# Performance work log

Hardware: AMD Instinct MI355X
Metric: run time of the kernel (lower is better)

Reference implementation:

```python
import jax, jax.numpy as jnp
import numpy as np

DIM = 256
HEADS = 8
BS = 8
N = 1024
NEG = -1.0e9


def setup_inputs() -> dict:
    key = jax.random.key(0)
    ks = jax.random.split(key, 8)
    feats = jax.random.normal(ks[0], (BS, N, DIM), dtype=jnp.float32)
    adj_mat = (jax.random.uniform(ks[1], (BS, N, N)) < 0.1).astype(jnp.float32)
    s = 1.0 / np.sqrt(DIM)
    fc_w = jax.random.normal(ks[2], (DIM, DIM * HEADS), dtype=jnp.float32) * s
    fc_b = jnp.zeros((DIM * HEADS,), dtype=jnp.float32)
    q_w = jax.random.normal(ks[3], (DIM, 1), dtype=jnp.float32) * s
    q_b = jnp.zeros((1,), dtype=jnp.float32)
    k_w = jax.random.normal(ks[4], (DIM, 1), dtype=jnp.float32) * s
    k_b = jnp.zeros((1,), dtype=jnp.float32)
    fp_w = jax.random.normal(ks[5], (DIM * HEADS, DIM), dtype=jnp.float32) * (1.0 / np.sqrt(DIM * HEADS))
    fp_b = jnp.zeros((DIM,), dtype=jnp.float32)
    return {"feats": feats, "adj_mat": adj_mat, "fc_w": fc_w, "fc_b": fc_b,
            "q_w": q_w, "q_b": q_b, "k_w": k_w, "k_b": k_b,
            "fp_w": fp_w, "fp_b": fp_b}


def reference(feats, adj_mat, fc_w, fc_b, q_w, q_b, k_w, k_b, fp_w, fp_b):
    bs, n, dim = feats.shape
    # [bs, N, heads*dim] -> [bs, heads, N, dim]
    feat_proj = (feats @ fc_w + fc_b).reshape(bs, n, HEADS, dim).transpose(0, 2, 1, 3)
    q = feat_proj @ q_w + q_b            # [bs, heads, N, 1]
    k = feat_proj @ k_w + k_b            # [bs, heads, N, 1]
    logits = q + jnp.swapaxes(k, -1, -2)  # additive scores [bs, heads, N, N]
    masked = logits + (1.0 - adj_mat[:, None]) * NEG
    masked = jax.nn.leaky_relu(masked, negative_slope=0.01)
    attn = jax.nn.softmax(masked, axis=-1)  # dropout is identity at eval
    out = attn @ feat_proj                   # [bs, heads, N, dim]
    out = out.transpose(0, 2, 1, 3).reshape(bs, n, HEADS * dim)
    out = out @ fp_w + fp_b + feats          # residual=True
    return jax.nn.sigmoid(out)
```

## Files before the change

kernel.cpp:

```cpp
#include <hip/hip_runtime.h>
#include <hip/hip_bf16.h>

typedef unsigned short u16;
typedef unsigned int u32;
typedef unsigned long long u64;
typedef __attribute__((ext_vector_type(8))) short short8;
typedef __attribute__((ext_vector_type(4))) float floatx4;
typedef const __attribute__((address_space(1))) void* gp_t;
typedef __attribute__((address_space(3))) void* sp_t;

static __device__ __forceinline__ u16 f2bf(float x) {
    __hip_bfloat16 h = __float2bfloat16(x);
    union { __hip_bfloat16 h; u16 u; } cv; cv.h = h; return cv.u;
}
static __device__ __forceinline__ float bf2f(u16 u) {
    union { u16 u; __hip_bfloat16 h; } cv; cv.u = u;
    return __bfloat162float(cv.h);
}

__global__ __launch_bounds__(256)
void k_prepall(const float* __restrict__ feats, const float* __restrict__ adj,
               const float* __restrict__ fc_w, const float* __restrict__ fc_b,
               const float* __restrict__ q_w, const float* __restrict__ q_b,
               const float* __restrict__ k_w, const float* __restrict__ k_b,
               const float* __restrict__ fp_w,
               u16* __restrict__ featsB, u64* __restrict__ m,
               u16* __restrict__ fcwT, u16* __restrict__ fpwT2,
               u16* __restrict__ W, float* __restrict__ C) {
    __shared__ float shbuf[64 * 65];
    int id = blockIdx.x, tid = threadIdx.x;
    if (id < 32768) {
        long i = (long)id * 256 + tid;
        float v = adj[i];
        u64 bm = __ballot(v > 0.f);
        if ((tid & 63) == 0) m[i >> 6] = bm;
        if (id < 2048) {
            int j = (id * 256 + tid) * 4;
            float4 f = *(const float4*)&feats[j];
            featsB[j + 0] = f2bf(f.x); featsB[j + 1] = f2bf(f.y);
            featsB[j + 2] = f2bf(f.z); featsB[j + 3] = f2bf(f.w);
        }
    } else if (id < 32896) {
        int t = id - 32768, bx = t & 31, by = t >> 5;
        float (*tt)[65] = (float(*)[65])shbuf;
        int c = tid & 63, r0 = tid >> 6;
        for (int rr = r0; rr < 64; rr += 4)
            tt[rr][c] = fc_w[(long)(by * 64 + rr) * 2048 + bx * 64 + c];
        __syncthreads();
        for (int rr = r0; rr < 64; rr += 4)
            fcwT[(long)(bx * 64 + rr) * 256 + by * 64 + c] = f2bf(tt[c][rr]);
    } else if (id < 34944) {
        int k = id - 32896;
        float v = fp_w[(long)k * 256 + tid];
        fpwT2[((long)(k >> 3)) * 2048 + tid * 8 + (k & 7)] = f2bf(v);
    } else {
        int t = id - 34944, x = t & 15, dq = t >> 4;
        int h = x & 7, kind = x >> 3;
        const float* w = kind ? k_w : q_w;
        float* ws_ = shbuf;
        ws_[tid] = w[tid];
        __syncthreads();
        int dl = tid >> 2, part = tid & 3;
        int d = dq * 64 + dl;
        const float* row = fc_w + (long)d * 2048 + h * 256 + part * 64;
        float a = 0.f;
        #pragma unroll 8
        for (int i = 0; i < 64; i++) a += row[i] * ws_[part * 64 + i];
        a += __shfl_xor(a, 1);
        a += __shfl_xor(a, 2);
        if (part == 0) W[(long)x * 256 + d] = f2bf(a);
        if (tid == 0 && dq == 0) {
            float cb = 0.f;
            const float* fb = fc_b + h * 256;
            for (int i = 0; i < 256; i++) cb += fb[i] * ws_[i];
            C[x] = cb + (kind ? k_b[0] : q_b[0]);
        }
    }
}

__global__ __launch_bounds__(256, 2)
void k_g1qk(const u16* __restrict__ A, const u16* __restrict__ Bt,
            const float* __restrict__ bias, u16* __restrict__ V2,
            const u16* __restrict__ Wb, const float* __restrict__ C,
            float* __restrict__ qo, float* __restrict__ ko) {
    __shared__ u16 As[128 * 40];
    __shared__ u16 Bs[128 * 40];
    int tid  = threadIdx.x;
    int wave = tid >> 6, lane = tid & 63;
    int q  = lane >> 4, n16 = lane & 15;

    if (blockIdx.y >= 16) {
        int blk = (blockIdx.y - 16) * 64 + blockIdx.x;
        int rowBase = blk * 64 + wave * 16;
        const u16* arow = Bt + (long)(rowBase + n16) * 256 + q * 8;
        const u16* brow = Wb + n16 * 256 + q * 8;
        floatx4 acc = {};
        #pragma unroll
        for (int k0 = 0; k0 < 256; k0 += 32) {
            short8 af = *(const short8*)&arow[k0];
            short8 bf = *(const short8*)&brow[k0];
            acc = __builtin_amdgcn_mfma_f32_16x16x32_bf16(af, bf, acc, 0, 0, 0);
        }
        float cc = C[n16];
        #pragma unroll
        for (int r = 0; r < 4; r++) {
            int gr = rowBase + q * 4 + r;
            int b = gr >> 10, nn = gr & 1023;
            float v = acc[r] + cc;
            if (n16 < 8) qo[((b * 8 + n16) << 10) + nn] = v;
            else         ko[((b * 8 + (n16 - 8)) << 10) + nn] = v;
        }
        return;
    }

    int rowBase = blockIdx.y * 128;
    int colBase = blockIdx.x * 128;
    int wr = wave >> 1, wc = wave & 1;
    floatx4 acc[4][4] = {};
    int sm = tid >> 2;
    int sk = (tid & 3) * 8;

    for (int k0 = 0; k0 < 256; k0 += 32) {
        int4 a0 = *(const int4*)&A[(long)(rowBase + sm) * 256 + k0 + sk];
        int4 a1 = *(const int4*)&A[(long)(rowBase + sm + 64) * 256 + k0 + sk];
        int4 b0 = *(const int4*)&Bt[(long)(colBase + sm) * 256 + k0 + sk];
        int4 b1 = *(const int4*)&Bt[(long)(colBase + sm + 64) * 256 + k0 + sk];
        __syncthreads();
        *(int4*)&As[sm * 40 + sk]        = a0;
        *(int4*)&As[(sm + 64) * 40 + sk] = a1;
        *(int4*)&Bs[sm * 40 + sk]        = b0;
        *(int4*)&Bs[(sm + 64) * 40 + sk] = b1;
        __syncthreads();
        short8 af[4], bfr[4];
        #pragma unroll
        for (int i = 0; i < 4; i++)
            af[i] = *(short8*)&As[(wr * 64 + i * 16 + n16) * 40 + q * 8];
        #pragma unroll
        for (int i = 0; i < 4; i++)
            bfr[i] = *(short8*)&Bs[(wc * 64 + i * 16 + n16) * 40 + q * 8];
        #pragma unroll
        for (int mi = 0; mi < 4; mi++)
            #pragma unroll
            for (int ni = 0; ni < 4; ni++)
                acc[mi][ni] = __builtin_amdgcn_mfma_f32_16x16x32_bf16(
                    af[mi], bfr[ni], acc[mi][ni], 0, 0, 0);
    }

    #pragma unroll
    for (int mi = 0; mi < 4; mi++) {
        #pragma unroll
        for (int r = 0; r < 4; r++) {
            int grow = rowBase + wr * 64 + mi * 16 + q * 4 + r;
            int h = grow >> 8, d = grow & 255;
            float bv = bias[grow];
            #pragma unroll
            for (int ni = 0; ni < 4; ni++) {
                int gcol = colBase + wc * 64 + ni * 16 + n16;
                int b = gcol >> 10, nn = gcol & 1023;
                V2[(((long)(b * 8 + h)) << 18) + (nn >> 3) * 2048 + d * 8 + (nn & 7)]
                    = f2bf(acc[mi][ni][r] + bv);
            }
        }
    }
}

__global__ __launch_bounds__(512)
__attribute__((amdgpu_waves_per_eu(4)))
void k_attn(const u32* __restrict__ maskW, const float* __restrict__ qv,
            const float* __restrict__ kv, const u16* __restrict__ fpjT2,
            u16* __restrict__ outh2) {
    __shared__ u16 As[2][128 * 40];
    __shared__ u16 Bs[2][4 * 256 * 8];
    __shared__ float qS[128], kS[1024], lsumS[512], rlS[128];

    int z = blockIdx.x;
    int b = z >> 3, h = z & 7;
    int i0 = blockIdx.y * 128;
    int tid = threadIdx.x;
    int wave = tid >> 6, lane = tid & 63;
    int wr = wave >> 2, wc = wave & 3;
    int q  = lane >> 4, n16 = lane & 15;

    if (tid < 256) *(float4*)&kS[tid * 4] = *(const float4*)&kv[(z << 10) + tid * 4];
    if (tid >= 256 && tid < 384) qS[tid - 256] = qv[(z << 10) + i0 + (tid - 256)];

    floatx4 acc[4][4] = {};
    int ar = tid >> 2;
    int jq = (tid & 3) * 8;
    const u32* mrow = maskW + (((long)(b << 10) + i0 + ar) << 5);
    const u16* Vbase = fpjT2 + ((long)z << 18);
    float lsum = 0.f;

    auto dma_v = [&](int k0, int p) {
        #pragma unroll
        for (int t = 0; t < 2; t++) {
            int s = wave * 2 + t;
            __builtin_amdgcn_global_load_lds(
                (gp_t)&Vbase[((k0 >> 3) + (s >> 2)) * 2048 + ((s & 3) * 64 + lane) * 8],
                (sp_t)&Bs[p][((s >> 2) * 256 + (s & 3) * 64 + lane) * 8],
                16, 0, 0);
        }
    };
    auto stage_p = [&](int k0, int p) {
        u32 mw = mrow[k0 >> 5] >> jq;
        float qi = qS[ar];
        float4 kA = *(const float4*)&kS[k0 + jq];
        float4 kB = *(const float4*)&kS[k0 + jq + 4];
        float kk[8] = {kA.x, kA.y, kA.z, kA.w, kB.x, kB.y, kB.z, kB.w};
        u32 pw[4];
        #pragma unroll
        for (int e2 = 0; e2 < 4; e2++) {
            float s0 = qi + kk[2 * e2];
            s0 = fmaxf(s0, 0.01f * s0);
            float p0 = ((mw >> (2 * e2)) & 1u) ? __expf(s0) : 0.f;
            float s1 = qi + kk[2 * e2 + 1];
            s1 = fmaxf(s1, 0.01f * s1);
            float p1 = ((mw >> (2 * e2 + 1)) & 1u) ? __expf(s1) : 0.f;
            lsum += p0 + p1;
            pw[e2] = __builtin_amdgcn_perm(__float_as_uint(p1), __float_as_uint(p0),
                                           0x07060302);
        }
        *(int4*)&As[p][ar * 40 + jq] = *(int4*)&pw[0];
    };

    __syncthreads();
    dma_v(0, 0);
    stage_p(0, 0);
    __syncthreads();

    for (int k0 = 0; k0 < 1024; k0 += 32) {
        int p = (k0 >> 5) & 1;
        short8 af[4], bfr[4];
        #pragma unroll
        for (int i = 0; i < 4; i++)
            af[i] = *(short8*)&As[p][(wr * 64 + i * 16 + n16) * 40 + q * 8];
        #pragma unroll
        for (int i = 0; i < 4; i++)
            bfr[i] = *(short8*)&Bs[p][(q * 256 + wc * 64 + i * 16 + n16) * 8];
        if (k0 + 32 < 1024) {
            dma_v(k0 + 32, p ^ 1);
            stage_p(k0 + 32, p ^ 1);
        }
        #pragma unroll
        for (int mi = 0; mi < 4; mi++)
            #pragma unroll
            for (int ni = 0; ni < 4; ni++)
                acc[mi][ni] = __builtin_amdgcn_mfma_f32_16x16x32_bf16(
                    af[mi], bfr[ni], acc[mi][ni], 0, 0, 0);
        __syncthreads();
    }

    lsumS[tid] = lsum;
    __syncthreads();
    if (tid < 128) {
        float l = lsumS[4 * tid] + lsumS[4 * tid + 1] +
                  lsumS[4 * tid + 2] + lsumS[4 * tid + 3];
        rlS[tid] = l > 0.f ? 1.f / l : 0.f;
    }
    __syncthreads();

    #pragma unroll
    for (int mi = 0; mi < 4; mi++) {
        #pragma unroll
        for (int r = 0; r < 4; r++) {
            int grow = wr * 64 + mi * 16 + q * 4 + r;
            float s = rlS[grow];
            long row = (long)(b * 1024 + i0 + grow);
            #pragma unroll
            for (int ni = 0; ni < 4; ni++) {
                int gcol = wc * 64 + ni * 16 + n16;
                outh2[((long)(h * 32 + (gcol >> 3)) << 16) + row * 8 + (gcol & 7)]
                    = f2bf(acc[mi][ni][r] * s);
            }
        }
    }
}

__global__ __launch_bounds__(256)
void k_g3(const u16* __restrict__ A2,
          const u16* __restrict__ B2,
          const float* __restrict__ bias,
          const float* __restrict__ resid,
          float* __restrict__ out) {
    __shared__ u16 As[2][8 * 64 * 8];
    __shared__ u16 Bs[2][8 * 32 * 8];
    int rowBase = blockIdx.x * 64;
    int colBase = blockIdx.y * 32;
    int tid = threadIdx.x, wave = tid >> 6, lane = tid & 63;
    int q = lane >> 4, n16 = lane & 15;
    floatx4 acc[2] = {};

    auto dma = [&](int k0, int p) {
        int kc = k0 >> 3;
        #pragma unroll
        for (int t = 0; t < 2; t++) {
            int c = wave + t * 4;
            __builtin_amdgcn_global_load_lds(
                (gp_t)&A2[(long)(kc + c) * 65536 + (rowBase + lane) * 8],
                (sp_t)&As[p][(c * 64 + lane) * 8], 16, 0, 0);
        }
        __builtin_amdgcn_global_load_lds(
            (gp_t)&B2[(long)(kc + wave * 2 + (lane >> 5)) * 2048
                      + (colBase + (lane & 31)) * 8],
            (sp_t)&Bs[p][(wave * 64 + lane) * 8], 16, 0, 0);
    };

    dma(0, 0);
    __syncthreads();
    for (int k0 = 0; k0 < 2048; k0 += 64) {
        int p = (k0 >> 6) & 1;
        short8 af[2], bfr[2][2];
        #pragma unroll
        for (int kf = 0; kf < 2; kf++) {
            af[kf] = *(short8*)&As[p][((kf * 4 + q) * 64 + wave * 16 + n16) * 8];
            #pragma unroll
            for (int nf = 0; nf < 2; nf++)
                bfr[kf][nf] = *(short8*)&Bs[p][((kf * 4 + q) * 32 + nf * 16 + n16) * 8];
        }
        if (k0 + 64 < 2048) dma(k0 + 64, p ^ 1);
        #pragma unroll
        for (int kf = 0; kf < 2; kf++)
            #pragma unroll
            for (int nf = 0; nf < 2; nf++)
                acc[nf] = __builtin_amdgcn_mfma_f32_16x16x32_bf16(
                    af[kf], bfr[kf][nf], acc[nf], 0, 0, 0);
        __syncthreads();
    }

    #pragma unroll
    for (int nf = 0; nf < 2; nf++) {
        #pragma unroll
        for (int r = 0; r < 4; r++) {
            int grow = rowBase + wave * 16 + q * 4 + r;
            int gcol = colBase + nf * 16 + n16;
            float v = acc[nf][r] + bias[gcol] + resid[(long)grow * 256 + gcol];
            out[(long)grow * 256 + gcol] = 1.f / (1.f + __expf(-v));
        }
    }
}

extern "C" void kernel_launch(void* const* d_in, const int* in_sizes, int n_in,
                              void* d_out, int out_size, void* d_ws, size_t ws_size,
                              hipStream_t stream) {
    const float* feats = (const float*)d_in[0];
    const float* adj   = (const float*)d_in[1];
    const float* fc_w  = (const float*)d_in[2];
    const float* fc_b  = (const float*)d_in[3];
    const float* q_w   = (const float*)d_in[4];
    const float* q_b   = (const float*)d_in[5];
    const float* k_w   = (const float*)d_in[6];
    const float* k_b   = (const float*)d_in[7];
    const float* fp_w  = (const float*)d_in[8];
    const float* fp_b  = (const float*)d_in[9];

    char* ws = (char*)d_ws;
    u16*   featsB = (u16*)ws;   ws += (size_t)2097152 * 2;
    u16*   fcwT   = (u16*)ws;   ws += (size_t)524288 * 2;
    u16*   fpwT2  = (u16*)ws;   ws += (size_t)524288 * 2;
    u16*   fpjT2  = (u16*)ws;   ws += (size_t)16777216 * 2;
    float* qv     = (float*)ws; ws += (size_t)65536 * 4;
    float* kv     = (float*)ws; ws += (size_t)65536 * 4;
    u16*   outh2  = (u16*)ws;   ws += (size_t)16777216 * 2;
    u64*   maskB  = (u64*)ws;   ws += (size_t)131072 * 8;
    u16*   Weff   = (u16*)ws;   ws += (size_t)4096 * 2;
    float* Ceff   = (float*)ws; ws += (size_t)16 * 4;

    k_prepall<<<35008, 256, 0, stream>>>(feats, adj, fc_w, fc_b, q_w, q_b,
                                         k_w, k_b, fp_w,
                                         featsB, maskB, fcwT, fpwT2, Weff, Ceff);

    k_g1qk<<<dim3(64, 18), 256, 0, stream>>>(fcwT, featsB, fc_b, fpjT2,
                                             Weff, Ceff, qv, kv);

    k_attn<<<dim3(64, 8), 512, 0, stream>>>((const u32*)maskB, qv, kv, fpjT2, outh2);

    k_g3<<<dim3(128, 8), 256, 0, stream>>>(outh2, fpwT2, fp_b, feats, (float*)d_out);
}
```

Measured before the change: 205.7 us.

## Repack operands into k-chunked layouts, use LDS DMA double buffering, retile output GEMM

The prep kernel now builds the adjacency bitmask with float4 loads and 16-bit writes per thread instead of wave ballots, cutting the block count sharply. It also stores feats, fc_w and fp_w in k-chunk-major bf16 layouts. The first GEMM switches to double-buffered global_load_lds DMA in place of register-staged LDS copies and drops its occupancy hint. The attention kernel prefetches the next step's mask and k values before the MFMA step, and the final GEMM moves to 64x64 tiles with a 2x2 wave layout. Together these aim to cut memory traffic and load latency across all four kernels, at the cost of a large multi-part change with new layout assumptions.

```diff
diff --git a/kernel.cpp b/kernel.cpp
--- a/kernel.cpp
+++ b/kernel.cpp
@@ -13,10 +13,6 @@
     __hip_bfloat16 h = __float2bfloat16(x);
     union { __hip_bfloat16 h; u16 u; } cv; cv.h = h; return cv.u;
 }
-static __device__ __forceinline__ float bf2f(u16 u) {
-    union { u16 u; __hip_bfloat16 h; } cv; cv.u = u;
-    return __bfloat162float(cv.h);
-}
 
 __global__ __launch_bounds__(256)
 void k_prepall(const float* __restrict__ feats, const float* __restrict__ adj,
@@ -24,43 +20,71 @@
                const float* __restrict__ q_w, const float* __restrict__ q_b,
                const float* __restrict__ k_w, const float* __restrict__ k_b,
                const float* __restrict__ fp_w,
-               u16* __restrict__ featsB, u64* __restrict__ m,
-               u16* __restrict__ fcwT, u16* __restrict__ fpwT2,
+               u16* __restrict__ feats2, u16* __restrict__ maskH,
+               u16* __restrict__ fcw2, u16* __restrict__ fpw2,
                u16* __restrict__ W, float* __restrict__ C) {
     __shared__ float shbuf[64 * 65];
-    int id = blockIdx.x, tid = threadIdx.x;
-    if (id < 32768) {
-        long i = (long)id * 256 + tid;
-        float v = adj[i];
-        u64 bm = __ballot(v > 0.f);
-        if ((tid & 63) == 0) m[i >> 6] = bm;
-        if (id < 2048) {
-            int j = (id * 256 + tid) * 4;
-            float4 f = *(const float4*)&feats[j];
-            featsB[j + 0] = f2bf(f.x); featsB[j + 1] = f2bf(f.y);
-            featsB[j + 2] = f2bf(f.z); featsB[j + 3] = f2bf(f.w);
-        }
-    } else if (id < 32896) {
-        int t = id - 32768, bx = t & 31, by = t >> 5;
+    int id = blockIdx.x, t = threadIdx.x;
+    if (id < 2048) {
+        long g = (long)id * 256 + t;
+        const float4* ap = (const float4*)adj + g * 4;
+        u32 mm = 0;
+        #pragma unroll
+        for (int w = 0; w < 4; w++) {
+            float4 f = ap[w];
+            mm |= (f.x > 0.f ? 1u : 0u) << (4 * w);
+            mm |= (f.y > 0.f ? 1u : 0u) << (4 * w + 1);
+            mm |= (f.z > 0.f ? 1u : 0u) << (4 * w + 2);
+            mm |= (f.w > 0.f ? 1u : 0u) << (4 * w + 3);
+        }
+        maskH[g] = (u16)mm;
+    } else if (id < 3072) {
+        int n = (id - 2048) * 8 + (t >> 5), c = t & 31;
+        const float* src = feats + (long)n * 256 + c * 8;
+        float4 f0 = *(const float4*)src, f1 = *(const float4*)(src + 4);
+        u16 tmp[8] = {f2bf(f0.x), f2bf(f0.y), f2bf(f0.z), f2bf(f0.w),
+                      f2bf(f1.x), f2bf(f1.y), f2bf(f1.z), f2bf(f1.w)};
+        *(int4*)&feats2[(long)c * 65536 + n * 8] = *(int4*)tmp;
+    } else if (id < 3200) {
+        int b = id - 3072, bx = b & 31, by = b >> 5;
         float (*tt)[65] = (float(*)[65])shbuf;
-        int c = tid & 63, r0 = tid >> 6;
+        int c = t & 63, r0 = t >> 6;
         for (int rr = r0; rr < 64; rr += 4)
             tt[rr][c] = fc_w[(long)(by * 64 + rr) * 2048 + bx * 64 + c];
         __syncthreads();
+        int hdl = t & 63;
+        #pragma unroll
+        for (int oo = 0; oo < 2; oo++) {
+            int o = (t >> 6) + oo * 4;
+            u16 tmp[8];
+            #pragma unroll
+            for (int e = 0; e < 8; e++) tmp[e] = f2bf(tt[o * 8 + e][hdl]);
+            *(int4*)&fcw2[(long)(by * 8 + o) * 16384 + (bx * 64 + hdl) * 8] = *(int4*)tmp;
+        }
+    } else if (id < 3328) {
+        int b = id - 3200, bx = b & 3, by = b >> 2;
+        float (*tt)[65] = (float(*)[65])shbuf;
+        int c = t & 63, r0 = t >> 6;
         for (int rr = r0; rr < 64; rr += 4)
-            fcwT[(long)(bx * 64 + rr) * 256 + by * 64 + c] = f2bf(tt[c][rr]);
-    } else if (id < 34944) {
-        int k = id - 32896;
-        float v = fp_w[(long)k * 256 + tid];
-        fpwT2[((long)(k >> 3)) * 2048 + tid * 8 + (k & 7)] = f2bf(v);
+            tt[rr][c] = fp_w[(long)(by * 64 + rr) * 256 + bx * 64 + c];
+        __syncthreads();
+        int cl = t & 63;
+        #pragma unroll
+        for (int oo = 0; oo < 2; oo++) {
+            int o = (t >> 6) + oo * 4;
+            u16 tmp[8];
+            #pragma unroll
+            for (int e = 0; e < 8; e++) tmp[e] = f2bf(tt[o * 8 + e][cl]);
+            *(int4*)&fpw2[(long)(by * 8 + o) * 2048 + (bx * 64 + cl) * 8] = *(int4*)tmp;
+        }
     } else {
-        int t = id - 34944, x = t & 15, dq = t >> 4;
+        int t2 = id - 3328, x = t2 & 15, dq = t2 >> 4;
         int h = x & 7, kind = x >> 3;
         const float* w = kind ? k_w : q_w;
         float* ws_ = shbuf;
-        ws_[tid] = w[tid];
-        __syncthreads();
-        int dl = tid >> 2, part = tid & 3;
+        ws_[t] = w[t];
+        __syncthreads();
+        int dl = t >> 2, part = t & 3;
         int d = dq * 64 + dl;
         const float* row = fc_w + (long)d * 2048 + h * 256 + part * 64;
         float a = 0.f;
@@ -69,7 +93,7 @@
         a += __shfl_xor(a, 1);
         a += __shfl_xor(a, 2);
         if (part == 0) W[(long)x * 256 + d] = f2bf(a);
-        if (tid == 0 && dq == 0) {
+        if (t == 0 && dq == 0) {
             float cb = 0.f;
             const float* fb = fc_b + h * 256;
             for (int i = 0; i < 256; i++) cb += fb[i] * ws_[i];
@@ -78,27 +102,23 @@
     }
 }
 
-__global__ __launch_bounds__(256, 2)
-void k_g1qk(const u16* __restrict__ A, const u16* __restrict__ Bt,
+__global__ __launch_bounds__(256)
+void k_g1qk(const u16* __restrict__ fcw2, const u16* __restrict__ feats2,
             const float* __restrict__ bias, u16* __restrict__ V2,
             const u16* __restrict__ Wb, const float* __restrict__ C,
             float* __restrict__ qo, float* __restrict__ ko) {
-    __shared__ u16 As[128 * 40];
-    __shared__ u16 Bs[128 * 40];
-    int tid  = threadIdx.x;
-    int wave = tid >> 6, lane = tid & 63;
-    int q  = lane >> 4, n16 = lane & 15;
+    int tid = threadIdx.x, wave = tid >> 6, lane = tid & 63;
+    int q = lane >> 4, n16 = lane & 15;
 
     if (blockIdx.y >= 16) {
         int blk = (blockIdx.y - 16) * 64 + blockIdx.x;
         int rowBase = blk * 64 + wave * 16;
-        const u16* arow = Bt + (long)(rowBase + n16) * 256 + q * 8;
-        const u16* brow = Wb + n16 * 256 + q * 8;
         floatx4 acc = {};
         #pragma unroll
         for (int k0 = 0; k0 < 256; k0 += 32) {
-            short8 af = *(const short8*)&arow[k0];
-            short8 bf = *(const short8*)&brow[k0];
+            short8 af = *(const short8*)&feats2[(long)((k0 >> 3) + q) * 65536
+                                                + (rowBase + n16) * 8];
+            short8 bf = *(const short8*)&Wb[n16 * 256 + k0 + q * 8];
             acc = __builtin_amdgcn_mfma_f32_16x16x32_bf16(af, bf, acc, 0, 0, 0);
         }
         float cc = C[n16];
@@ -113,37 +133,45 @@
         return;
     }
 
+    __shared__ u16 As[2][4 * 128 * 8];
+    __shared__ u16 Bs[2][4 * 128 * 8];
     int rowBase = blockIdx.y * 128;
     int colBase = blockIdx.x * 128;
     int wr = wave >> 1, wc = wave & 1;
     floatx4 acc[4][4] = {};
-    int sm = tid >> 2;
-    int sk = (tid & 3) * 8;
-
+
+    auto dma = [&](int k0, int p) {
+        int kc = k0 >> 3;
+        #pragma unroll
+        for (int r = 0; r < 2; r++) {
+            __builtin_amdgcn_global_load_lds(
+                (gp_t)&fcw2[(long)(kc + wave) * 16384 + (rowBase + r * 64 + lane) * 8],
+                (sp_t)&As[p][(wave * 128 + r * 64 + lane) * 8], 16, 0, 0);
+            __builtin_amdgcn_global_load_lds(
+                (gp_t)&feats2[(long)(kc + wave) * 65536 + (colBase + r * 64 + lane) * 8],
+                (sp_t)&Bs[p][(wave * 128 + r * 64 + lane) * 8], 16, 0, 0);
+        }
+    };
+
+    dma(0, 0);
+    __syncthreads();
     for (int k0 = 0; k0 < 256; k0 += 32) {
-        int4 a0 = *(const int4*)&A[(long)(rowBase + sm) * 256 + k0 + sk];
-        int4 a1 = *(const int4*)&A[(long)(rowBase + sm + 64) * 256 + k0 + sk];
-        int4 b0 = *(const int4*)&Bt[(long)(colBase + sm) * 256 + k0 + sk];
-        int4 b1 = *(const int4*)&Bt[(long)(colBase + sm + 64) * 256 + k0 + sk];
-        __syncthreads();
-        *(int4*)&As[sm * 40 + sk]        = a0;
-        *(int4*)&As[(sm + 64) * 40 + sk] = a1;
-        *(int4*)&Bs[sm * 40 + sk]        = b0;
-        *(int4*)&Bs[(sm + 64) * 40 + sk] = b1;
-        __syncthreads();
+        int p = (k0 >> 5) & 1;
         short8 af[4], bfr[4];
         #pragma unroll
         for (int i = 0; i < 4; i++)
-            af[i] = *(short8*)&As[(wr * 64 + i * 16 + n16) * 40 + q * 8];
+            af[i] = *(short8*)&As[p][(q * 128 + wr * 64 + i * 16 + n16) * 8];
         #pragma unroll
         for (int i = 0; i < 4; i++)
-            bfr[i] = *(short8*)&Bs[(wc * 64 + i * 16 + n16) * 40 + q * 8];
+            bfr[i] = *(short8*)&Bs[p][(q * 128 + wc * 64 + i * 16 + n16) * 8];
+        if (k0 + 32 < 256) dma(k0 + 32, p ^ 1);
         #pragma unroll
         for (int mi = 0; mi < 4; mi++)
             #pragma unroll
             for (int ni = 0; ni < 4; ni++)
                 acc[mi][ni] = __builtin_amdgcn_mfma_f32_16x16x32_bf16(
                     af[mi], bfr[ni], acc[mi][ni], 0, 0, 0);
+        __syncthreads();
     }
 
     #pragma unroll
@@ -201,11 +229,11 @@
                 16, 0, 0);
         }
     };
-    auto stage_p = [&](int k0, int p) {
-        u32 mw = mrow[k0 >> 5] >> jq;
-        float qi = qS[ar];
-        float4 kA = *(const float4*)&kS[k0 + jq];
-        float4 kB = *(const float4*)&kS[k0 + jq + 4];
+
+    __syncthreads();
+    float qi = qS[ar];
+
+    auto stage_p = [&](int p, u32 mw, float4 kA, float4 kB) {
         float kk[8] = {kA.x, kA.y, kA.z, kA.w, kB.x, kB.y, kB.z, kB.w};
         u32 pw[4];
         #pragma unroll
@@ -223,13 +251,21 @@
         *(int4*)&As[p][ar * 40 + jq] = *(int4*)&pw[0];
     };
 
-    __syncthreads();
-    dma_v(0, 0);
-    stage_p(0, 0);
+    {
+        u32 mw0 = mrow[0] >> jq;
+        float4 kA0 = *(const float4*)&kS[jq];
+        float4 kB0 = *(const float4*)&kS[jq + 4];
+        dma_v(0, 0);
+        stage_p(0, mw0, kA0, kB0);
+    }
     __syncthreads();
 
     for (int k0 = 0; k0 < 1024; k0 += 32) {
         int p = (k0 >> 5) & 1;
+        int kn = (k0 + 32 < 1024) ? k0 + 32 : 0;
+        u32 mw = mrow[kn >> 5] >> jq;
+        float4 kA = *(const float4*)&kS[kn + jq];
+        float4 kB = *(const float4*)&kS[kn + jq + 4];
         short8 af[4], bfr[4];
         #pragma unroll
         for (int i = 0; i < 4; i++)
@@ -239,7 +275,7 @@
             bfr[i] = *(short8*)&Bs[p][(q * 256 + wc * 64 + i * 16 + n16) * 8];
         if (k0 + 32 < 1024) {
             dma_v(k0 + 32, p ^ 1);
-            stage_p(k0 + 32, p ^ 1);
+            stage_p(p ^ 1, mw, kA, kB);
         }
         #pragma unroll
         for (int mi = 0; mi < 4; mi++)
@@ -283,58 +319,63 @@
           const float* __restrict__ resid,
           float* __restrict__ out) {
     __shared__ u16 As[2][8 * 64 * 8];
-    __shared__ u16 Bs[2][8 * 32 * 8];
+    __shared__ u16 Bs[2][8 * 64 * 8];
     int rowBase = blockIdx.x * 64;
-    int colBase = blockIdx.y * 32;
+    int colBase = blockIdx.y * 64;
     int tid = threadIdx.x, wave = tid >> 6, lane = tid & 63;
+    int wr = wave >> 1, wc = wave & 1;
     int q = lane >> 4, n16 = lane & 15;
-    floatx4 acc[2] = {};
+    floatx4 acc[2][2] = {};
 
     auto dma = [&](int k0, int p) {
         int kc = k0 >> 3;
         #pragma unroll
-        for (int t = 0; t < 2; t++) {
-            int c = wave + t * 4;
+        for (int s = 0; s < 2; s++) {
+            int c = wave + s * 4;
             __builtin_amdgcn_global_load_lds(
                 (gp_t)&A2[(long)(kc + c) * 65536 + (rowBase + lane) * 8],
                 (sp_t)&As[p][(c * 64 + lane) * 8], 16, 0, 0);
-        }
-        __builtin_amdgcn_global_load_lds(
-            (gp_t)&B2[(long)(kc + wave * 2 + (lane >> 5)) * 2048
-                      + (colBase + (lane & 31)) * 8],
-            (sp_t)&Bs[p][(wave * 64 + lane) * 8], 16, 0, 0);
+            __builtin_amdgcn_global_load_lds(
+                (gp_t)&B2[(long)(kc + c) * 2048 + (colBase + lane) * 8],
+                (sp_t)&Bs[p][(c * 64 + lane) * 8], 16, 0, 0);
+        }
     };
 
     dma(0, 0);
     __syncthreads();
     for (int k0 = 0; k0 < 2048; k0 += 64) {
         int p = (k0 >> 6) & 1;
-        short8 af[2], bfr[2][2];
-        #pragma unroll
-        for (int kf = 0; kf < 2; kf++) {
-            af[kf] = *(short8*)&As[p][((kf * 4 + q) * 64 + wave * 16 + n16) * 8];
-            #pragma unroll
-            for (int nf = 0; nf < 2; nf++)
-                bfr[kf][nf] = *(short8*)&Bs[p][((kf * 4 + q) * 32 + nf * 16 + n16) * 8];
-        }
+        short8 af[2][2], bfr[2][2];
+        #pragma unroll
+        for (int kf = 0; kf < 2; kf++)
+            #pragma unroll
+            for (int i = 0; i < 2; i++) {
+                af[kf][i]  = *(short8*)&As[p][((kf * 4 + q) * 64 + wr * 32 + i * 16 + n16) * 8];
+                bfr[kf][i] = *(short8*)&Bs[p][((kf * 4 + q) * 64 + wc * 32 + i * 16 + n16) * 8];
+            }
         if (k0 + 64 < 2048) dma(k0 + 64, p ^ 1);
         #pragma unroll
         for (int kf = 0; kf < 2; kf++)
             #pragma unroll
-            for (int nf = 0; nf < 2; nf++)
-                acc[nf] = __builtin_amdgcn_mfma_f32_16x16x32_bf16(
-                    af[kf], bfr[kf][nf], acc[nf], 0, 0, 0);
+            for (int mi = 0; mi < 2; mi++)
+                #pragma unroll
+                for (int ni = 0; ni < 2; ni++)
+                    acc[mi][ni] = __builtin_amdgcn_mfma_f32_16x16x32_bf16(
+                        af[kf][mi], bfr[kf][ni], acc[mi][ni], 0, 0, 0);
         __syncthreads();
     }
 
     #pragma unroll
-    for (int nf = 0; nf < 2; nf++) {
+    for (int mi = 0; mi < 2; mi++) {
         #pragma unroll
         for (int r = 0; r < 4; r++) {
-            int grow = rowBase + wave * 16 + q * 4 + r;
-            int gcol = colBase + nf * 16 + n16;
-            float v = acc[nf][r] + bias[gcol] + resid[(long)grow * 256 + gcol];
-            out[(long)grow * 256 + gcol] = 1.f / (1.f + __expf(-v));
+            int grow = rowBase + wr * 32 + mi * 16 + q * 4 + r;
+            #pragma unroll
+            for (int ni = 0; ni < 2; ni++) {
+                int gcol = colBase + wc * 32 + ni * 16 + n16;
+                float v = acc[mi][ni][r] + bias[gcol] + resid[(long)grow * 256 + gcol];
+                out[(long)grow * 256 + gcol] = 1.f / (1.f + __expf(-v));
+            }
         }
     }
 }
@@ -354,9 +395,9 @@
     const float* fp_b  = (const float*)d_in[9];
 
     char* ws = (char*)d_ws;
-    u16*   featsB = (u16*)ws;   ws += (size_t)2097152 * 2;
-    u16*   fcwT   = (u16*)ws;   ws += (size_t)524288 * 2;
-    u16*   fpwT2  = (u16*)ws;   ws += (size_t)524288 * 2;
+    u16*   feats2 = (u16*)ws;   ws += (size_t)2097152 * 2;
+    u16*   fcw2   = (u16*)ws;   ws += (size_t)524288 * 2;
+    u16*   fpw2   = (u16*)ws;   ws += (size_t)524288 * 2;
     u16*   fpjT2  = (u16*)ws;   ws += (size_t)16777216 * 2;
     float* qv     = (float*)ws; ws += (size_t)65536 * 4;
     float* kv     = (float*)ws; ws += (size_t)65536 * 4;
@@ -365,14 +406,14 @@
     u16*   Weff   = (u16*)ws;   ws += (size_t)4096 * 2;
     float* Ceff   = (float*)ws; ws += (size_t)16 * 4;
 
-    k_prepall<<<35008, 256, 0, stream>>>(feats, adj, fc_w, fc_b, q_w, q_b,
-                                         k_w, k_b, fp_w,
-                                         featsB, maskB, fcwT, fpwT2, Weff, Ceff);
-
-    k_g1qk<<<dim3(64, 18), 256, 0, stream>>>(fcwT, featsB, fc_b, fpjT2,
+    k_prepall<<<3392, 256, 0, stream>>>(feats, adj, fc_w, fc_b, q_w, q_b,
+                                        k_w, k_b, fp_w,
+                                        feats2, (u16*)maskB, fcw2, fpw2, Weff, Ceff);
+
+    k_g1qk<<<dim3(64, 18), 256, 0, stream>>>(fcw2, feats2, fc_b, fpjT2,
                                              Weff, Ceff, qv, kv);
 
     k_attn<<<dim3(64, 8), 512, 0, stream>>>((const u32*)maskB, qv, kv, fpjT2, outh2);
 
-    k_g3<<<dim3(128, 8), 256, 0, stream>>>(outh2, fpwT2, fp_b, feats, (float*)d_out);
-}
+    k_g3<<<dim3(128, 4), 256, 0, stream>>>(outh2, fpw2, fp_b, feats, (float*)d_out);
+}
```

New measurement: 195.0 us. -5.2%, faster.
